# Kernel tuning notes

Hardware: AMD Instinct MI355X
Metric: run time of the kernel (lower is better)

The kernel has to match this reference:

```python
import jax, jax.numpy as jnp
import numpy as np

EMBED = 768
HEAD_DIM = 64  # 768 // 12
SEQ = 4096
BATCH = 4


def setup_inputs() -> dict:
    key = jax.random.key(0)
    ks = jax.random.split(key, 7)
    s = 1.0 / np.sqrt(EMBED)
    return {
        "hidden_state": jax.random.normal(ks[0], (BATCH, SEQ, EMBED), dtype=jnp.float32),
        "Wq": jax.random.uniform(ks[1], (EMBED, HEAD_DIM), jnp.float32, -s, s),
        "bq": jax.random.uniform(ks[2], (HEAD_DIM,), jnp.float32, -s, s),
        "Wk": jax.random.uniform(ks[3], (EMBED, HEAD_DIM), jnp.float32, -s, s),
        "bk": jax.random.uniform(ks[4], (HEAD_DIM,), jnp.float32, -s, s),
        "Wv": jax.random.uniform(ks[5], (EMBED, HEAD_DIM), jnp.float32, -s, s),
        "bv": jax.random.uniform(ks[6], (HEAD_DIM,), jnp.float32, -s, s),
    }


def reference(hidden_state, Wq, bq, Wk, bk, Wv, bv):
    # single-head causal attention: QK^T / sqrt(d) -> causal mask -> softmax -> V
    q = hidden_state @ Wq + bq  # [B, S, d]
    k = hidden_state @ Wk + bk
    v = hidden_state @ Wv + bv
    scale = 1.0 / jnp.sqrt(jnp.asarray(HEAD_DIM, dtype=q.dtype))
    scores = jnp.einsum("bqd,bkd->bqk", q, k) * scale  # [B, S, S]
    S = scores.shape[-1]
    causal = jnp.tril(jnp.ones((S, S), dtype=bool))  # tril buffer, mask==0 -> -inf
    scores = jnp.where(causal, scores, -jnp.inf)
    weights = jax.nn.softmax(scores, axis=-1)
    return jnp.einsum("bqk,bkd->bqd", weights, v)  # [B, S, d]
```

## Files before the change

### kernel.cpp

```cpp
#include <hip/hip_runtime.h>
#include <stdint.h>

#define EMBED 768
#define HD 64
#define SEQ 4096
#define BATCH 4
#define NROW (BATCH * SEQ)
#define NSTRIP (NROW / 16)
#define KSPLIT 4

typedef __bf16 bf16x8 __attribute__((ext_vector_type(8)));
typedef __bf16 bf16x4 __attribute__((ext_vector_type(4)));
typedef float f32x4 __attribute__((ext_vector_type(4)));

__global__ __launch_bounds__(256)
void wconv_kernel(const float* __restrict__ Wq, const float* __restrict__ Wk,
                  const float* __restrict__ Wv, __bf16* __restrict__ wT) {
    int id = blockIdx.x * 256 + threadIdx.x;
    int c = id / EMBED, k = id - c * EMBED;
    const float* W = (c < 64) ? Wq : (c < 128) ? Wk : Wv;
    wT[id] = (__bf16)W[(size_t)k * HD + (c & 63)];
}

__global__ __launch_bounds__(64)
void qkv_gemm_kernel(const float* __restrict__ hidden, const __bf16* __restrict__ wT,
                     const float* __restrict__ bq, const float* __restrict__ bk,
                     const float* __restrict__ bv,
                     __bf16* __restrict__ qo, __bf16* __restrict__ ko,
                     __bf16* __restrict__ vto) {
    const int m0 = blockIdx.x * 16;
    const int lane = threadIdx.x, lr = lane & 15, lg = lane >> 4;

    f32x4 acc[12];
    #pragma unroll
    for (int n = 0; n < 12; ++n) acc[n] = (f32x4){0.f, 0.f, 0.f, 0.f};

    const float* hrow = hidden + (size_t)(m0 + lr) * EMBED + lg * 8;
    const __bf16* wbase = wT + lg * 8;

    for (int k0 = 0; k0 < EMBED; k0 += 64) {
        bf16x8 a[2];
        #pragma unroll
        for (int ks = 0; ks < 2; ++ks) {
            float4 h0 = *(const float4*)(hrow + k0 + ks * 32);
            float4 h1 = *(const float4*)(hrow + k0 + ks * 32 + 4);
            bf16x8 t;
            t[0] = (__bf16)h0.x; t[1] = (__bf16)h0.y; t[2] = (__bf16)h0.z; t[3] = (__bf16)h0.w;
            t[4] = (__bf16)h1.x; t[5] = (__bf16)h1.y; t[6] = (__bf16)h1.z; t[7] = (__bf16)h1.w;
            a[ks] = t;
        }
        #pragma unroll
        for (int n = 0; n < 12; ++n) {
            #pragma unroll
            for (int ks = 0; ks < 2; ++ks) {
                bf16x8 bb = *(const bf16x8*)(wbase + (size_t)(n * 16 + lr) * EMBED + k0 + ks * 32);
                acc[n] = __builtin_amdgcn_mfma_f32_16x16x32_bf16(a[ks], bb, acc[n], 0, 0, 0);
            }
        }
    }

    const int row0 = m0 + lg * 4;
    #pragma unroll
    for (int n = 0; n < 4; ++n) {
        const float b1 = bq[n * 16 + lr];
        const float b2 = bk[n * 16 + lr];
        const float b3 = bv[n * 16 + lr];
        #pragma unroll
        for (int r = 0; r < 4; ++r) {
            qo[(size_t)(row0 + r) * HD + n * 16 + lr] = (__bf16)(acc[n][r] + b1);
            ko[(size_t)(row0 + r) * HD + n * 16 + lr] = (__bf16)(acc[n + 4][r] + b2);
        }
        bf16x4 pv;
        pv[0] = (__bf16)(acc[n + 8][0] + b3);
        pv[1] = (__bf16)(acc[n + 8][1] + b3);
        pv[2] = (__bf16)(acc[n + 8][2] + b3);
        pv[3] = (__bf16)(acc[n + 8][3] + b3);
        *(bf16x4*)&vto[(size_t)(n * 16 + lr) * NROW + row0] = pv;
    }
}

__global__ __launch_bounds__(64)
void attn_kernel(const __bf16* __restrict__ qg, const __bf16* __restrict__ kg,
                 const __bf16* __restrict__ vtg,
                 float* __restrict__ opart, float* __restrict__ ml) {
    __shared__ __bf16 p_lds[16][72];

    const int bid   = blockIdx.x;
    const int s     = (NSTRIP - 1) - (bid >> 2);
    const int split = bid & 3;
    const int b     = s & 3;
    const int q0    = (s >> 2) * 16;
    const int lane = threadIdx.x, lr = lane & 15, lg = lane >> 4;

    const int nk    = q0 + 16;
    const int chunk = ((nk + KSPLIT * 64 - 1) / (KSPLIT * 64)) * 64;
    const int kb    = split * chunk;
    const int ke    = (kb + chunk < nk) ? (kb + chunk) : nk;

    float* mlp = ml + ((size_t)s * KSPLIT + split) * 32;
    if (kb >= ke) {
        if (lane < 16) mlp[16 + lane] = 0.f;
        return;
    }

    const __bf16* qb = qg  + (size_t)b * SEQ * HD;
    const __bf16* kp = kg  + (size_t)b * SEQ * HD;
    const __bf16* vb = vtg + (size_t)b * SEQ;

    const bf16x8 qf0 = *(const bf16x8*)&qb[(q0 + lr) * HD + lg * 8];
    const bf16x8 qf1 = *(const bf16x8*)&qb[(q0 + lr) * HD + 32 + lg * 8];

    f32x4 acc[4];
    const f32x4 zero4 = {0.f, 0.f, 0.f, 0.f};
    #pragma unroll
    for (int n = 0; n < 4; ++n) acc[n] = zero4;
    float m[4], lsum[4];
    #pragma unroll
    for (int r = 0; r < 4; ++r) { m[r] = -INFINITY; lsum[r] = 0.f; }

    const float sc = 0.18033688011112042f;

    for (int kb0 = kb; kb0 < ke; kb0 += 64) {
        f32x4 sj[4];
        #pragma unroll
        for (int j = 0; j < 4; ++j) {
            bf16x8 kf0 = *(const bf16x8*)&kp[(size_t)(kb0 + j * 16 + lr) * HD + lg * 8];
            bf16x8 kf1 = *(const bf16x8*)&kp[(size_t)(kb0 + j * 16 + lr) * HD + 32 + lg * 8];
            f32x4 z = zero4;
            z = __builtin_amdgcn_mfma_f32_16x16x32_bf16(qf0, kf0, z, 0, 0, 0);
            z = __builtin_amdgcn_mfma_f32_16x16x32_bf16(qf1, kf1, z, 0, 0, 0);
            sj[j] = z;
        }

        float t[4][4];
        #pragma unroll
        for (int j = 0; j < 4; ++j)
            #pragma unroll
            for (int r = 0; r < 4; ++r) t[j][r] = sj[j][r] * sc;

        if (kb0 + 63 > q0) {
            #pragma unroll
            for (int j = 0; j < 4; ++j)
                #pragma unroll
                for (int r = 0; r < 4; ++r)
                    if (kb0 + j * 16 + lr > q0 + lg * 4 + r) t[j][r] = -1e30f;
        }

        float mx[4];
        #pragma unroll
        for (int r = 0; r < 4; ++r)
            mx[r] = fmaxf(fmaxf(t[0][r], t[1][r]), fmaxf(t[2][r], t[3][r]));
        #pragma unroll
        for (int off = 1; off < 16; off <<= 1)
            #pragma unroll
            for (int r = 0; r < 4; ++r) mx[r] = fmaxf(mx[r], __shfl_xor(mx[r], off));

        float p[4][4], rs[4], so[4];
        #pragma unroll
        for (int r = 0; r < 4; ++r) {
            const float nm = fmaxf(m[r], mx[r]);
            so[r] = __builtin_exp2f(m[r] - nm);
            m[r] = nm;
            float a = 0.f;
            #pragma unroll
            for (int j = 0; j < 4; ++j) { p[j][r] = __builtin_exp2f(t[j][r] - nm); a += p[j][r]; }
            rs[r] = a;
        }
        #pragma unroll
        for (int off = 1; off < 16; off <<= 1)
            #pragma unroll
            for (int r = 0; r < 4; ++r) rs[r] += __shfl_xor(rs[r], off);
        #pragma unroll
        for (int r = 0; r < 4; ++r) lsum[r] = lsum[r] * so[r] + rs[r];
        #pragma unroll
        for (int n = 0; n < 4; ++n)
            #pragma unroll
            for (int r = 0; r < 4; ++r) acc[n][r] *= so[r];

        #pragma unroll
        for (int j = 0; j < 4; ++j)
            #pragma unroll
            for (int r = 0; r < 4; ++r)
                p_lds[lg * 4 + r][j * 16 + lr] = (__bf16)p[j][r];
        asm volatile("s_waitcnt lgkmcnt(0)" ::: "memory");
        const bf16x8 pa0 = *(const bf16x8*)&p_lds[lr][lg * 8];
        const bf16x8 pa1 = *(const bf16x8*)&p_lds[lr][32 + lg * 8];
        #pragma unroll
        for (int n = 0; n < 4; ++n) {
            bf16x8 vf0 = *(const bf16x8*)&vb[(size_t)(n * 16 + lr) * NROW + kb0 + lg * 8];
            acc[n] = __builtin_amdgcn_mfma_f32_16x16x32_bf16(pa0, vf0, acc[n], 0, 0, 0);
            bf16x8 vf1 = *(const bf16x8*)&vb[(size_t)(n * 16 + lr) * NROW + kb0 + 32 + lg * 8];
            acc[n] = __builtin_amdgcn_mfma_f32_16x16x32_bf16(pa1, vf1, acc[n], 0, 0, 0);
        }
        asm volatile("" ::: "memory");
    }

    float* Op = opart + ((size_t)s * KSPLIT + split) * (16 * 64);
    #pragma unroll
    for (int n = 0; n < 4; ++n)
        #pragma unroll
        for (int r = 0; r < 4; ++r)
            Op[(size_t)(lg * 4 + r) * 64 + n * 16 + lr] = acc[n][r];
    if (lr == 0) {
        #pragma unroll
        for (int r = 0; r < 4; ++r) {
            const float lout = (m[r] > -1e29f) ? lsum[r] : 0.f;
            mlp[lg * 4 + r]      = m[r];
            mlp[16 + lg * 4 + r] = lout;
        }
    }
}

__global__ __launch_bounds__(256)
void reduce_kernel(const float* __restrict__ opart, const float* __restrict__ ml,
                   float* __restrict__ out) {
    const int e   = blockIdx.x * 256 + threadIdx.x;
    const int col = e & 63;
    const int row = e >> 6;
    const int b   = row >> 12;
    const int sq  = row & (SEQ - 1);
    const int s   = ((sq >> 4) << 2) | b;
    const int r   = sq & 15;
    const int nk  = (sq & ~15) + 16;
    const int chunk = ((nk + KSPLIT * 64 - 1) / (KSPLIT * 64)) * 64;
    const int nsp   = (nk + chunk - 1) / chunk;

    float M = -INFINITY, ls = 0.f, o = 0.f;
    for (int sp = 0; sp < nsp; ++sp) {
        const float* mlp = ml + ((size_t)s * KSPLIT + sp) * 32;
        const float lv = mlp[16 + r];
        if (lv > 0.f) {
            const float mv = mlp[r];
            const float nm = fmaxf(M, mv);
            const float f0 = __builtin_exp2f(M - nm);
            const float f1 = __builtin_exp2f(mv - nm);
            const float ov = opart[((size_t)s * KSPLIT + sp) * (16 * 64) + (size_t)r * 64 + col];
            o  = o * f0 + f1 * ov;
            ls = ls * f0 + f1 * lv;
            M = nm;
        }
    }
    out[e] = o / ls;
}

extern "C" void kernel_launch(void* const* d_in, const int* in_sizes, int n_in,
                              void* d_out, int out_size, void* d_ws, size_t ws_size,
                              hipStream_t stream) {
    const float* hidden = (const float*)d_in[0];
    const float* Wq = (const float*)d_in[1];
    const float* bq = (const float*)d_in[2];
    const float* Wk = (const float*)d_in[3];
    const float* bk = (const float*)d_in[4];
    const float* Wv = (const float*)d_in[5];
    const float* bv = (const float*)d_in[6];

    __bf16* qbuf  = (__bf16*)d_ws;
    __bf16* kbuf  = qbuf + (size_t)NROW * HD;
    __bf16* vtbuf = kbuf + (size_t)NROW * HD;
    __bf16* wT    = vtbuf + (size_t)NROW * HD;
    float*  opart = (float*)(wT + (size_t)192 * EMBED);
    float*  ml    = opart + (size_t)NSTRIP * KSPLIT * 16 * 64;

    wconv_kernel<<<(192 * EMBED) / 256, 256, 0, stream>>>(Wq, Wk, Wv, wT);

    qkv_gemm_kernel<<<NROW / 16, 64, 0, stream>>>(
        hidden, wT, bq, bk, bv, qbuf, kbuf, vtbuf);

    attn_kernel<<<NSTRIP * KSPLIT, 64, 0, stream>>>(
        qbuf, kbuf, vtbuf, opart, ml);

    reduce_kernel<<<(NROW * HD) / 256, 256, 0, stream>>>(opart, ml, (float*)d_out);
}
```

Baseline: 207.6 us.

## Group four query strips per attention block and split QKV GEMM by matrix

The attention kernel now runs 256-thread blocks in which four waves each handle a 16-row strip of a 64-row query band, sharing a K split range. KSPLIT rises to 8, with partial outputs and max/sum laid out per band. The QKV projection grid gains a second dimension so each block computes only one of Q, K or V, cutting accumulator registers at the cost of re-reading hidden rows three times. The aim is better occupancy and shared K/V cache locality across waves, but it adds more partials for the reduce kernel and leaves per-wave work imbalance inside a band.

```diff
diff --git a/kernel.cpp b/kernel.cpp
--- a/kernel.cpp
+++ b/kernel.cpp
@@ -6,8 +6,8 @@
 #define SEQ 4096
 #define BATCH 4
 #define NROW (BATCH * SEQ)
-#define NSTRIP (NROW / 16)
-#define KSPLIT 4
+#define NBAND (NROW / 64)
+#define KSPLIT 8
 
 typedef __bf16 bf16x8 __attribute__((ext_vector_type(8)));
 typedef __bf16 bf16x4 __attribute__((ext_vector_type(4)));
@@ -28,15 +28,16 @@
                      const float* __restrict__ bv,
                      __bf16* __restrict__ qo, __bf16* __restrict__ ko,
                      __bf16* __restrict__ vto) {
-    const int m0 = blockIdx.x * 16;
+    const int mat = blockIdx.y;
+    const int m0  = blockIdx.x * 16;
     const int lane = threadIdx.x, lr = lane & 15, lg = lane >> 4;
 
-    f32x4 acc[12];
-    #pragma unroll
-    for (int n = 0; n < 12; ++n) acc[n] = (f32x4){0.f, 0.f, 0.f, 0.f};
-
-    const float* hrow = hidden + (size_t)(m0 + lr) * EMBED + lg * 8;
-    const __bf16* wbase = wT + lg * 8;
+    f32x4 acc[4];
+    #pragma unroll
+    for (int n = 0; n < 4; ++n) acc[n] = (f32x4){0.f, 0.f, 0.f, 0.f};
+
+    const float*  hrow  = hidden + (size_t)(m0 + lr) * EMBED + lg * 8;
+    const __bf16* wbase = wT + (size_t)mat * 64 * EMBED + lg * 8;
 
     for (int k0 = 0; k0 < EMBED; k0 += 64) {
         bf16x8 a[2];
@@ -44,13 +45,13 @@
         for (int ks = 0; ks < 2; ++ks) {
             float4 h0 = *(const float4*)(hrow + k0 + ks * 32);
             float4 h1 = *(const float4*)(hrow + k0 + ks * 32 + 4);
-            bf16x8 t;
-            t[0] = (__bf16)h0.x; t[1] = (__bf16)h0.y; t[2] = (__bf16)h0.z; t[3] = (__bf16)h0.w;
-            t[4] = (__bf16)h1.x; t[5] = (__bf16)h1.y; t[6] = (__bf16)h1.z; t[7] = (__bf16)h1.w;
-            a[ks] = t;
-        }
-        #pragma unroll
-        for (int n = 0; n < 12; ++n) {
+            bf16x8 tv;
+            tv[0] = (__bf16)h0.x; tv[1] = (__bf16)h0.y; tv[2] = (__bf16)h0.z; tv[3] = (__bf16)h0.w;
+            tv[4] = (__bf16)h1.x; tv[5] = (__bf16)h1.y; tv[6] = (__bf16)h1.z; tv[7] = (__bf16)h1.w;
+            a[ks] = tv;
+        }
+        #pragma unroll
+        for (int n = 0; n < 4; ++n) {
             #pragma unroll
             for (int ks = 0; ks < 2; ++ks) {
                 bf16x8 bb = *(const bf16x8*)(wbase + (size_t)(n * 16 + lr) * EMBED + k0 + ks * 32);
@@ -59,47 +60,61 @@
         }
     }
 
+    const float* bias = (mat == 0) ? bq : (mat == 1) ? bk : bv;
     const int row0 = m0 + lg * 4;
-    #pragma unroll
-    for (int n = 0; n < 4; ++n) {
-        const float b1 = bq[n * 16 + lr];
-        const float b2 = bk[n * 16 + lr];
-        const float b3 = bv[n * 16 + lr];
-        #pragma unroll
-        for (int r = 0; r < 4; ++r) {
-            qo[(size_t)(row0 + r) * HD + n * 16 + lr] = (__bf16)(acc[n][r] + b1);
-            ko[(size_t)(row0 + r) * HD + n * 16 + lr] = (__bf16)(acc[n + 4][r] + b2);
-        }
-        bf16x4 pv;
-        pv[0] = (__bf16)(acc[n + 8][0] + b3);
-        pv[1] = (__bf16)(acc[n + 8][1] + b3);
-        pv[2] = (__bf16)(acc[n + 8][2] + b3);
-        pv[3] = (__bf16)(acc[n + 8][3] + b3);
-        *(bf16x4*)&vto[(size_t)(n * 16 + lr) * NROW + row0] = pv;
-    }
-}
-
-__global__ __launch_bounds__(64)
+    if (mat < 2) {
+        __bf16* out = (mat == 0) ? qo : ko;
+        #pragma unroll
+        for (int n = 0; n < 4; ++n) {
+            const float bb = bias[n * 16 + lr];
+            #pragma unroll
+            for (int r = 0; r < 4; ++r)
+                out[(size_t)(row0 + r) * HD + n * 16 + lr] = (__bf16)(acc[n][r] + bb);
+        }
+    } else {
+        #pragma unroll
+        for (int n = 0; n < 4; ++n) {
+            const float bb = bias[n * 16 + lr];
+            bf16x4 pv;
+            pv[0] = (__bf16)(acc[n][0] + bb);
+            pv[1] = (__bf16)(acc[n][1] + bb);
+            pv[2] = (__bf16)(acc[n][2] + bb);
+            pv[3] = (__bf16)(acc[n][3] + bb);
+            *(bf16x4*)&vto[(size_t)(n * 16 + lr) * NROW + row0] = pv;
+        }
+    }
+}
+
+__global__ __launch_bounds__(256)
 void attn_kernel(const __bf16* __restrict__ qg, const __bf16* __restrict__ kg,
                  const __bf16* __restrict__ vtg,
                  float* __restrict__ opart, float* __restrict__ ml) {
-    __shared__ __bf16 p_lds[16][72];
-
-    const int bid   = blockIdx.x;
-    const int s     = (NSTRIP - 1) - (bid >> 2);
-    const int split = bid & 3;
-    const int b     = s & 3;
-    const int q0    = (s >> 2) * 16;
-    const int lane = threadIdx.x, lr = lane & 15, lg = lane >> 4;
-
-    const int nk    = q0 + 16;
-    const int chunk = ((nk + KSPLIT * 64 - 1) / (KSPLIT * 64)) * 64;
-    const int kb    = split * chunk;
-    const int ke    = (kb + chunk < nk) ? (kb + chunk) : nk;
-
-    float* mlp = ml + ((size_t)s * KSPLIT + split) * 32;
+    __shared__ __bf16 p_lds[4][16][72];
+
+    const int bid = blockIdx.x;
+    const int gi  = bid >> 3;
+    const int sp  = bid & (KSPLIT - 1);
+    const int t   = 63 - (gi >> 2);
+    const int b   = gi & 3;
+    const int q0b = t * 64;
+    const int nkb = q0b + 64;
+    const int chunk = ((nkb + 511) >> 9) << 6;
+    const int kb = sp * chunk;
+
+    const int w    = threadIdx.x >> 6;
+    const int lane = threadIdx.x & 63, lr = lane & 15, lg = lane >> 4;
+    const int q0 = q0b + w * 16;
+    const int nk = q0 + 16;
+    const int ke = (kb + chunk < nk) ? (kb + chunk) : nk;
+
+    float* mlp = ml + ((size_t)gi * KSPLIT + sp) * 128;
+    const int rb = w * 16 + lg * 4;
+
     if (kb >= ke) {
-        if (lane < 16) mlp[16 + lane] = 0.f;
+        if (lr == 0) {
+            #pragma unroll
+            for (int r = 0; r < 4; ++r) mlp[64 + rb + r] = 0.f;
+        }
         return;
     }
 
@@ -132,24 +147,24 @@
             sj[j] = z;
         }
 
-        float t[4][4];
+        float tt[4][4];
         #pragma unroll
         for (int j = 0; j < 4; ++j)
             #pragma unroll
-            for (int r = 0; r < 4; ++r) t[j][r] = sj[j][r] * sc;
+            for (int r = 0; r < 4; ++r) tt[j][r] = sj[j][r] * sc;
 
         if (kb0 + 63 > q0) {
             #pragma unroll
             for (int j = 0; j < 4; ++j)
                 #pragma unroll
                 for (int r = 0; r < 4; ++r)
-                    if (kb0 + j * 16 + lr > q0 + lg * 4 + r) t[j][r] = -1e30f;
+                    if (kb0 + j * 16 + lr > q0 + lg * 4 + r) tt[j][r] = -1e30f;
         }
 
         float mx[4];
         #pragma unroll
         for (int r = 0; r < 4; ++r)
-            mx[r] = fmaxf(fmaxf(t[0][r], t[1][r]), fmaxf(t[2][r], t[3][r]));
+            mx[r] = fmaxf(fmaxf(tt[0][r], tt[1][r]), fmaxf(tt[2][r], tt[3][r]));
         #pragma unroll
         for (int off = 1; off < 16; off <<= 1)
             #pragma unroll
@@ -163,7 +178,7 @@
             m[r] = nm;
             float a = 0.f;
             #pragma unroll
-            for (int j = 0; j < 4; ++j) { p[j][r] = __builtin_exp2f(t[j][r] - nm); a += p[j][r]; }
+            for (int j = 0; j < 4; ++j) { p[j][r] = __builtin_exp2f(tt[j][r] - nm); a += p[j][r]; }
             rs[r] = a;
         }
         #pragma unroll
@@ -181,10 +196,10 @@
         for (int j = 0; j < 4; ++j)
             #pragma unroll
             for (int r = 0; r < 4; ++r)
-                p_lds[lg * 4 + r][j * 16 + lr] = (__bf16)p[j][r];
+                p_lds[w][lg * 4 + r][j * 16 + lr] = (__bf16)p[j][r];
         asm volatile("s_waitcnt lgkmcnt(0)" ::: "memory");
-        const bf16x8 pa0 = *(const bf16x8*)&p_lds[lr][lg * 8];
-        const bf16x8 pa1 = *(const bf16x8*)&p_lds[lr][32 + lg * 8];
+        const bf16x8 pa0 = *(const bf16x8*)&p_lds[w][lr][lg * 8];
+        const bf16x8 pa1 = *(const bf16x8*)&p_lds[w][lr][32 + lg * 8];
         #pragma unroll
         for (int n = 0; n < 4; ++n) {
             bf16x8 vf0 = *(const bf16x8*)&vb[(size_t)(n * 16 + lr) * NROW + kb0 + lg * 8];
@@ -195,18 +210,17 @@
         asm volatile("" ::: "memory");
     }
 
-    float* Op = opart + ((size_t)s * KSPLIT + split) * (16 * 64);
+    float* Op = opart + (size_t)(gi * KSPLIT + sp) * (64 * 64);
     #pragma unroll
     for (int n = 0; n < 4; ++n)
         #pragma unroll
         for (int r = 0; r < 4; ++r)
-            Op[(size_t)(lg * 4 + r) * 64 + n * 16 + lr] = acc[n][r];
+            Op[(size_t)(rb + r) * 64 + n * 16 + lr] = acc[n][r];
     if (lr == 0) {
         #pragma unroll
         for (int r = 0; r < 4; ++r) {
-            const float lout = (m[r] > -1e29f) ? lsum[r] : 0.f;
-            mlp[lg * 4 + r]      = m[r];
-            mlp[16 + lg * 4 + r] = lout;
+            mlp[rb + r]      = m[r];
+            mlp[64 + rb + r] = (m[r] > -1e29f) ? lsum[r] : 0.f;
         }
     }
 }
@@ -219,22 +233,23 @@
     const int row = e >> 6;
     const int b   = row >> 12;
     const int sq  = row & (SEQ - 1);
-    const int s   = ((sq >> 4) << 2) | b;
-    const int r   = sq & 15;
-    const int nk  = (sq & ~15) + 16;
-    const int chunk = ((nk + KSPLIT * 64 - 1) / (KSPLIT * 64)) * 64;
-    const int nsp   = (nk + chunk - 1) / chunk;
+    const int t   = sq >> 6;
+    const int gi  = (63 - t) * 4 + b;
+    const int r64 = sq & 63;
+    const int nkb = (t + 1) * 64;
+    const int chunk = ((nkb + 511) >> 9) << 6;
+    const int nsp   = (nkb + chunk - 1) / chunk;
 
     float M = -INFINITY, ls = 0.f, o = 0.f;
     for (int sp = 0; sp < nsp; ++sp) {
-        const float* mlp = ml + ((size_t)s * KSPLIT + sp) * 32;
-        const float lv = mlp[16 + r];
+        const size_t base = (size_t)gi * KSPLIT + sp;
+        const float lv = ml[base * 128 + 64 + r64];
         if (lv > 0.f) {
-            const float mv = mlp[r];
+            const float mv = ml[base * 128 + r64];
             const float nm = fmaxf(M, mv);
             const float f0 = __builtin_exp2f(M - nm);
             const float f1 = __builtin_exp2f(mv - nm);
-            const float ov = opart[((size_t)s * KSPLIT + sp) * (16 * 64) + (size_t)r * 64 + col];
+            const float ov = opart[base * (64 * 64) + (size_t)r64 * 64 + col];
             o  = o * f0 + f1 * ov;
             ls = ls * f0 + f1 * lv;
             M = nm;
@@ -259,14 +274,14 @@
     __bf16* vtbuf = kbuf + (size_t)NROW * HD;
     __bf16* wT    = vtbuf + (size_t)NROW * HD;
     float*  opart = (float*)(wT + (size_t)192 * EMBED);
-    float*  ml    = opart + (size_t)NSTRIP * KSPLIT * 16 * 64;
+    float*  ml    = opart + (size_t)NBAND * KSPLIT * 64 * 64;
 
     wconv_kernel<<<(192 * EMBED) / 256, 256, 0, stream>>>(Wq, Wk, Wv, wT);
 
-    qkv_gemm_kernel<<<NROW / 16, 64, 0, stream>>>(
+    qkv_gemm_kernel<<<dim3(NROW / 16, 3), 64, 0, stream>>>(
         hidden, wT, bq, bk, bv, qbuf, kbuf, vtbuf);
 
-    attn_kernel<<<NSTRIP * KSPLIT, 64, 0, stream>>>(
+    attn_kernel<<<NBAND * KSPLIT, 256, 0, stream>>>(
         qbuf, kbuf, vtbuf, opart, ml);
 
     reduce_kernel<<<(NROW * HD) / 256, 256, 0, stream>>>(opart, ml, (float*)d_out);
```

Result: slower. 225.4 us (+8.6%).
